# Optimization experiments

Measured on AMD Instinct MI355X. Metric: run time of the kernel, lower is better.

Reference implementation:

```python
import jax, jax.numpy as jnp
import numpy as np

DT = 1.0 / 120.0  # hard-coded in the original SystemModel / EKF
N_TRAJ, T = 2048, 512
COV = np.array([2.5e-07, 2.5e-07, 0.0091, 2e-10, 1e-07, 0.01, 0.1], dtype=np.float32)


def _dynamics(s, friction, damping):
    # 6-dim puck state: [x, y, dx, dy, theta, dtheta]
    # Table damping (linear drag) + friction (smoothed Coulomb) act on linear velocity,
    # matching the SystemModel(tableDamping, tableFriction, dt=1/120) free-motion step.
    x, y, dx, dy, th, dth = s
    dx2 = dx - DT * (damping * dx + friction * jnp.tanh(100.0 * dx))
    dy2 = dy - DT * (damping * dy + friction * jnp.tanh(100.0 * dy))
    return jnp.stack([x + DT * dx, y + DT * dy, dx2, dy2, th + DT * dth, dth])


def _ekf_losses(measurements, init_state, dyna_params, Q, R, P0):
    friction, damping = dyna_params[0], dyna_params[1]
    dt_ = measurements.dtype
    H = jnp.zeros((3, 6), dt_).at[0, 0].set(1.0).at[1, 1].set(1.0).at[2, 4].set(1.0)
    I6 = jnp.eye(6, dtype=dt_)
    f = lambda s: _dynamics(s, friction, damping)
    Jf = jax.jacfwd(f)

    def step(carry, z):
        s, P = carry
        # --- predict ---
        s_pred = f(s)
        F = Jf(s)                      # 6x6 Jacobian of dynamics
        P_pred = F @ P @ F.T + Q
        # --- update ---
        y = z - H @ s_pred             # 3-dim innovation
        S = H @ P_pred @ H.T + R       # 3x3 innovation covariance
        S_inv = jnp.linalg.inv(S)
        K = P_pred @ H.T @ S_inv       # 6x3 Kalman gain
        s_new = s_pred + K @ y
        P_new = (I6 - K @ H) @ P_pred
        # per-point loss: det(S) (via slogdet as in the original) + Mahalanobis term
        sign, logdet = jnp.linalg.slogdet(S)
        loss = sign * jnp.exp(logdet) + y @ S_inv @ y
        return (s_new, P_new), loss

    def run(z_seq, s0):
        _, losses = jax.lax.scan(step, (s0, P0), z_seq)
        return losses

    return jax.vmap(run)(measurements, init_state).reshape(-1)


def setup_inputs() -> dict:
    key = jax.random.key(0)
    k1, k2 = jax.random.split(key, 2)
    measurements = jax.random.normal(k1, (N_TRAJ, T, 3), dtype=jnp.float32)
    init_state = jax.random.normal(k2, (N_TRAJ, 6), dtype=jnp.float32)
    # dyna_params = [tableFriction, tableDamping, restitution, rimFriction]
    dyna_params = jnp.array([0.1, 0.3, 0.8, 0.1], dtype=jnp.float32)
    cov = jnp.asarray(COV)
    R = jnp.diag(cov[:3])
    Q = jnp.diag(jnp.array([cov[3], cov[3], cov[4], cov[4], cov[5], cov[6]], dtype=jnp.float32))
    P0 = jnp.eye(6, dtype=jnp.float32) * 0.01
    return {"measurements": measurements, "init_state": init_state,
            "dyna_params": dyna_params, "Q": Q, "R": R, "P0": P0}


def reference(measurements, init_state, dyna_params, Q, R, P0):
    return _ekf_losses(measurements, init_state, dyna_params, Q, R, P0)
```

## Files before the change

### kernel.cpp

```cpp
#include <hip/hip_runtime.h>
#include <math.h>


#define TRIPLES 21
#define TILE    32
#define SMS     35

__device__ __forceinline__ float frcp(float x) { return __builtin_amdgcn_rcpf(x); }

__global__ __launch_bounds__(64, 1) void ekf_kernel(
    const float* __restrict__ meas,
    const float* __restrict__ init_state,
    const float* __restrict__ dyna,
    const float* __restrict__ Qm,
    const float* __restrict__ Rm,
    const float* __restrict__ P0m,
    float* __restrict__ out,
    int n_traj, int T)
{
    __shared__ float2 sSM[66 * SMS];

    const int lane  = threadIdx.x;
    const int k     = lane / 3;
    const int j     = lane - 3 * k;
    const int traj0 = blockIdx.x * TRIPLES;
    const int kk    = (k < TRIPLES) ? k : (TRIPLES - 1);
    const int traj  = traj0 + kk;
    const int traj_eff = (traj < n_traj) ? traj : (n_traj - 1);

    const int NT = T / TILE;
    const int T3 = 3 * T;

    const float DTc = 1.0f / 120.0f;
    const float Cc  = 288.53900817779268f;
    const float fric = dyna[0], damp = dyna[1];
    const bool  lin = (j == 2);
    const float ca  = lin ? 1.0f : (1.0f - DTc * damp);
    const float cf  = lin ? 0.0f : (DTc * fric);
    const float cb  = 100.0f * cf;
    const float ca2 = ca - cb;
    const int pi = (j == 0) ? 0 : (j == 1) ? 1 : 4;
    const int vi = pi + 2;
    const float qp = Qm[pi * 7], qv = Qm[vi * 7], qc = Qm[pi * 6 + vi];
    const float r   = Rm[j * 4];
    const float nr2 = -r * r;
    const float w0  = r + r + qp;
    float p02 = P0m[pi * 6 + vi], p22 = P0m[vi * 7];
    float w   = P0m[pi * 7] + qp + r;
    float pos = init_state[traj_eff * 6 + pi];
    float vel = init_state[traj_eff * 6 + vi];

    const int fhi  = lane >> 5;
    const int ftw  = lane & 31;
    const int fsm0 = 3 * fhi * SMS + ftw;
    const int fob0 = (traj0 + fhi) * T + ftw;

    const float* __restrict__ zlane = meas + (size_t)traj_eff * T3 + j;

    float zA[TILE], zB[TILE];
    #pragma unroll
    for (int tl = 0; tl < TILE; ++tl) zA[tl] = zlane[3 * tl];

#define EKF_PHASE(ZC, ZN, TIDX)                                              \
    do {                                                                     \
        const int tile_ = (TIDX);                                            \
        const int nt_   = (tile_ + 1 < NT) ? (tile_ + 1) : tile_;            \
        const float* __restrict__ znp_ = zlane + 96 * nt_;                   \
        _Pragma("unroll")                                                    \
        for (int tl = 0; tl < TILE; ++tl) ZN[tl] = znp_[3 * tl];             \
        float Sv[TILE], Mv[TILE];                                            \
        _Pragma("unroll")                                                    \
        for (int tl = 0; tl < TILE; ++tl) {                                  \
            const float z    = ZC[tl];                                       \
            const float e    = exp2f(Cc * vel);                              \
            const float ie   = frcp(e + 1.0f);                               \
            const float tx   = fmaf(-2.0f, ie, 1.0f);                        \
            const float t2   = tx * tx;                                      \
            const float u    = fmaf(DTc, p22, p02);                          \
            const float pu   = p02 + u;                                      \
            const float S    = fmaf(DTc, pu, w);             \
            const float rs   = frcp(S);                                      \
            const float sp   = fmaf(DTc, vel, pos);                          \
            const float yv   = z - sp;                                       \
            const float rsy  = rs * yv;                                      \
            const float a    = fmaf(cb, t2, ca2);                            \
            const float pp02 = fmaf(a, u, qc);                               \
            const float ap   = a * p22;                                      \
            const float pp22 = fmaf(ap, a, qv);                              \
            const float sv   = fmaf(-cf, tx, ca * vel);                      \
            vel = fmaf(pp02, rsy, sv);                                       \
            const float pp00 = S - r;                                        \
            pos = fmaf(pp00, rsy, sp);                                       \
            w   = fmaf(nr2, rs, w0);                                         \
            const float k1   = pp02 * rs;                                    \
            p02 = r * k1;                                                    \
            p22 = fmaf(-k1, pp02, pp22);                                     \
            Sv[tl] = S;                                                      \
            Mv[tl] = yv * rsy;                                               \
        }                                                                    \
              \
        float2* __restrict__ smr_ = &sSM[lane * SMS];                        \
        _Pragma("unroll")                                                    \
        for (int tl = 0; tl < TILE; ++tl)                                    \
            smr_[tl] = make_float2(Sv[tl], Mv[tl]);                          \
                \
        const int tb_ = tile_ * TILE;                                        \
        _Pragma("unroll")                                                    \
        for (int rr = 0; rr < 11; ++rr) {                                    \
            const int ck_ = 2 * rr + fhi;                                    \
            const bool ok_ = (rr * 64 + lane < TRIPLES * TILE) &&            \
                             (traj0 + ck_ < n_traj);                         \
            const int sa_ = fsm0 + rr * (6 * SMS);                           \
            const float2 a0_ = sSM[sa_];                                     \
            const float2 a1_ = sSM[sa_ + SMS];                               \
            const float2 a2_ = sSM[sa_ + 2 * SMS];                           \
            const float loss_ = (a0_.x * a1_.x) * a2_.x +                    \
                                (a0_.y + a1_.y + a2_.y);                     \
            if (ok_) out[(size_t)(fob0 + 2 * rr * T + tb_)] = loss_;         \
        }                                                                    \
    } while (0)

    #pragma unroll 1
    for (int th = 0; th < NT; th += 2) {
        EKF_PHASE(zA, zB, th);
        if (th + 1 < NT) EKF_PHASE(zB, zA, th + 1);
    }

#undef EKF_PHASE
}

extern "C" void kernel_launch(void* const* d_in, const int* in_sizes, int n_in,
                              void* d_out, int out_size, void* d_ws, size_t ws_size,
                              hipStream_t stream) {
    const float* meas = (const float*)d_in[0];
    const float* init_state = (const float*)d_in[1];
    const float* dyna = (const float*)d_in[2];
    const float* Qm  = (const float*)d_in[3];
    const float* Rm  = (const float*)d_in[4];
    const float* P0m = (const float*)d_in[5];
    float* out = (float*)d_out;

    const int n_traj = in_sizes[1] / 6;
    const int T = in_sizes[0] / (n_traj * 3);

    const int grid = (n_traj + TRIPLES - 1) / TRIPLES;
    ekf_kernel<<<grid, 64, 0, stream>>>(meas, init_state, dyna, Qm, Rm, P0m,
                                        out, n_traj, T);
}
```

Baseline: 117.8 us.

## Scale state by exp2 constant, simplify tanh derivative, vectorize LDS staging and stores

Keeps position and velocity pre-scaled by the exp2 constant, so the per-step multiply before exp2f disappears and the Mahalanobis term is rescaled once at output time. The tanh derivative is rewritten as ie - ie^2 and the tanh value is folded into an fma on ie, which shortens the serial dependency chain in the recurrence. The loss staging buffer changes from float2 to float4 rows, and each lane writes two adjacent outputs as a float2, halving LDS ops and global store instructions. Scaling by about 288 adds some risk of float rounding and range differences. The theta lane now indexes slot 5 for its velocity, which appears to fix the Q/P0 indexing.

Measured after the change: 111.9 us. -5.1%, faster.

```diff
diff --git a/kernel.cpp b/kernel.cpp
--- a/kernel.cpp
+++ b/kernel.cpp
@@ -4,7 +4,7 @@
 
 #define TRIPLES 21
 #define TILE    32
-#define SMS     35
+#define SMS4    17
 
 __device__ __forceinline__ float frcp(float x) { return __builtin_amdgcn_rcpf(x); }
 
@@ -18,7 +18,7 @@
     float* __restrict__ out,
     int n_traj, int T)
 {
-    __shared__ float2 sSM[66 * SMS];
+    __shared__ float4 sSM4[72 * SMS4];
 
     const int lane  = threadIdx.x;
     const int k     = lane / 3;
@@ -33,27 +33,30 @@
 
     const float DTc = 1.0f / 120.0f;
     const float Cc  = 288.53900817779268f;
+    const float invCc2 = 1.0f / (Cc * Cc);
     const float fric = dyna[0], damp = dyna[1];
     const bool  lin = (j == 2);
     const float ca  = lin ? 1.0f : (1.0f - DTc * damp);
     const float cf  = lin ? 0.0f : (DTc * fric);
     const float cb  = 100.0f * cf;
-    const float ca2 = ca - cb;
+    const float m4cb  = -4.0f * cb;
+    const float cf2Cc = 2.0f * (cf * Cc);
+    const float mcfCc = -(cf * Cc);
     const int pi = (j == 0) ? 0 : (j == 1) ? 1 : 4;
-    const int vi = pi + 2;
+    const int vi = lin ? 5 : (pi + 2);
     const float qp = Qm[pi * 7], qv = Qm[vi * 7], qc = Qm[pi * 6 + vi];
     const float r   = Rm[j * 4];
     const float nr2 = -r * r;
     const float w0  = r + r + qp;
     float p02 = P0m[pi * 6 + vi], p22 = P0m[vi * 7];
     float w   = P0m[pi * 7] + qp + r;
-    float pos = init_state[traj_eff * 6 + pi];
-    float vel = init_state[traj_eff * 6 + vi];
+    float posC = Cc * init_state[traj_eff * 6 + pi];
+    float xv   = Cc * init_state[traj_eff * 6 + vi];
 
-    const int fhi  = lane >> 5;
-    const int ftw  = lane & 31;
-    const int fsm0 = 3 * fhi * SMS + ftw;
-    const int fob0 = (traj0 + fhi) * T + ftw;
+    const int fh = lane >> 4;
+    const int tw = lane & 15;
+    const int fb0 = (3 * fh) * SMS4 + tw;
+    float* const obase = out + (size_t)(traj0 + fh) * T + 2 * tw;
 
     const float* __restrict__ zlane = meas + (size_t)traj_eff * T3 + j;
 
@@ -72,51 +75,52 @@
         _Pragma("unroll")                                                    \
         for (int tl = 0; tl < TILE; ++tl) {                                  \
             const float z    = ZC[tl];                                       \
-            const float e    = exp2f(Cc * vel);                              \
+            const float e    = exp2f(xv);                    \
             const float ie   = frcp(e + 1.0f);                               \
-            const float tx   = fmaf(-2.0f, ie, 1.0f);                        \
-            const float t2   = tx * tx;                                      \
+            const float t    = fmaf(-ie, ie, ie);             \
+            const float a    = fmaf(m4cb, t, ca);                            \
             const float u    = fmaf(DTc, p22, p02);                          \
-            const float pu   = p02 + u;                                      \
-            const float S    = fmaf(DTc, pu, w);             \
+            const float wp   = fmaf(DTc, p02, w);                            \
+            const float S    = fmaf(DTc, u, wp);             \
             const float rs   = frcp(S);                                      \
-            const float sp   = fmaf(DTc, vel, pos);                          \
-            const float yv   = z - sp;                                       \
-            const float rsy  = rs * yv;                                      \
-            const float a    = fmaf(cb, t2, ca2);                            \
+            const float spC  = fmaf(DTc, xv, posC);                          \
+            const float yvC  = fmaf(Cc, z, -spC);                            \
+            const float rsyC = rs * yvC;                                     \
             const float pp02 = fmaf(a, u, qc);                               \
             const float ap   = a * p22;                                      \
             const float pp22 = fmaf(ap, a, qv);                              \
-            const float sv   = fmaf(-cf, tx, ca * vel);                      \
-            vel = fmaf(pp02, rsy, sv);                                       \
+            const float sviC = fmaf(ca, xv, mcfCc);                          \
+            const float svC  = fmaf(cf2Cc, ie, sviC);                        \
+            xv   = fmaf(pp02, rsyC, svC);                                    \
             const float pp00 = S - r;                                        \
-            pos = fmaf(pp00, rsy, sp);                                       \
-            w   = fmaf(nr2, rs, w0);                                         \
-            const float k1   = pp02 * rs;                                    \
+            posC = fmaf(pp00, rsyC, spC);                                    \
+            w    = fmaf(nr2, rs, w0);                                        \
+            const float k1 = pp02 * rs;                                      \
             p02 = r * k1;                                                    \
             p22 = fmaf(-k1, pp02, pp22);                                     \
             Sv[tl] = S;                                                      \
-            Mv[tl] = yv * rsy;                                               \
+            Mv[tl] = yvC * rsyC;        \
         }                                                                    \
-              \
-        float2* __restrict__ smr_ = &sSM[lane * SMS];                        \
+                       \
         _Pragma("unroll")                                                    \
-        for (int tl = 0; tl < TILE; ++tl)                                    \
-            smr_[tl] = make_float2(Sv[tl], Mv[tl]);                          \
-                \
+        for (int h = 0; h < TILE / 2; ++h)                                   \
+            sSM4[lane * SMS4 + h] =                                          \
+                make_float4(Sv[2*h], Mv[2*h], Sv[2*h+1], Mv[2*h+1]);         \
+                      \
         const int tb_ = tile_ * TILE;                                        \
         _Pragma("unroll")                                                    \
-        for (int rr = 0; rr < 11; ++rr) {                                    \
-            const int ck_ = 2 * rr + fhi;                                    \
-            const bool ok_ = (rr * 64 + lane < TRIPLES * TILE) &&            \
-                             (traj0 + ck_ < n_traj);                         \
-            const int sa_ = fsm0 + rr * (6 * SMS);                           \
-            const float2 a0_ = sSM[sa_];                                     \
-            const float2 a1_ = sSM[sa_ + SMS];                               \
-            const float2 a2_ = sSM[sa_ + 2 * SMS];                           \
-            const float loss_ = (a0_.x * a1_.x) * a2_.x +                    \
-                                (a0_.y + a1_.y + a2_.y);                     \
-            if (ok_) out[(size_t)(fob0 + 2 * rr * T + tb_)] = loss_;         \
+        for (int rr = 0; rr < 6; ++rr) {                                     \
+            const int ck_ = 4 * rr + fh;                                     \
+            const bool ok_ = (ck_ < TRIPLES) && (traj0 + ck_ < n_traj);      \
+            const float4 a0_ = sSM4[fb0 + 204 * rr];                         \
+            const float4 a1_ = sSM4[fb0 + 204 * rr + SMS4];                  \
+            const float4 a2_ = sSM4[fb0 + 204 * rr + 2 * SMS4];              \
+            const float l0_ = fmaf(a0_.y + a1_.y + a2_.y, invCc2,            \
+                                   (a0_.x * a1_.x) * a2_.x);                 \
+            const float l1_ = fmaf(a0_.w + a1_.w + a2_.w, invCc2,            \
+                                   (a0_.z * a1_.z) * a2_.z);                 \
+            if (ok_) *(float2*)(obase + tb_ + rr * (4 * T)) =                \
+                make_float2(l0_, l1_);                                       \
         }                                                                    \
     } while (0)
 
```
